# Kernel tuning notes

Hardware: AMD Instinct MI355X
Metric: run time of the kernel (lower is better)

The kernel has to match this reference:

```python
import jax, jax.numpy as jnp
import numpy as np

DIM = 1024
HEADS = 8
HEAD_DIM = DIM // HEADS
FFN = 4096
B, N = 32, 1024
EPS = 1e-5


def layer_norm(x, g, b):
    mu = jnp.mean(x, axis=-1, keepdims=True)
    var = jnp.mean(jnp.square(x - mu), axis=-1, keepdims=True)
    return (x - mu) * jax.lax.rsqrt(var + EPS) * g + b


def setup_inputs() -> dict:
    key = jax.random.key(0)
    ks = jax.random.split(key, 10)
    s = 0.02
    return {
        "x": jax.random.normal(ks[0], (B, N, DIM), dtype=jnp.float32),
        "haltingscore": jnp.zeros((B, N), dtype=jnp.float32),
        "Wq": jax.random.normal(ks[1], (DIM, DIM), dtype=jnp.float32) * s,
        "Wkv": jax.random.normal(ks[2], (DIM, 2 * DIM), dtype=jnp.float32) * s,
        "Wp": jax.random.normal(ks[3], (DIM, DIM), dtype=jnp.float32) * s,
        "bp": jnp.zeros((DIM,), dtype=jnp.float32),
        "W1": jax.random.normal(ks[4], (DIM, FFN), dtype=jnp.float32) * s,
        "b1": jnp.zeros((FFN,), dtype=jnp.float32),
        "W2": jax.random.normal(ks[5], (FFN, DIM), dtype=jnp.float32) * s,
        "b2": jnp.zeros((DIM,), dtype=jnp.float32),
        "ln1_g": jnp.ones((DIM,), dtype=jnp.float32),
        "ln1_b": jnp.zeros((DIM,), dtype=jnp.float32),
        "ln2_g": jnp.ones((DIM,), dtype=jnp.float32),
        "ln2_b": jnp.zeros((DIM,), dtype=jnp.float32),
    }


def reference(x, haltingscore, Wq, Wkv, Wp, bp, W1, b1, W2, b2,
              ln1_g, ln1_b, ln2_g, ln2_b):
    b, n, c = x.shape
    scale = HEAD_DIM ** -0.5
    # ---- EfficientAttention (explicit QK^T softmax V) ----
    q = (x @ Wq).reshape(b, n, HEADS, HEAD_DIM).transpose(0, 2, 1, 3)  # bhnd
    kv = (x @ Wkv).reshape(b, n, 2, HEADS, HEAD_DIM).transpose(2, 0, 3, 1, 4)
    k, v = kv[0], kv[1]                                               # bhnd
    attn = jax.nn.softmax(jnp.einsum('bhnd,bhmd->bhnm', q, k) * scale, axis=-1)
    o = jnp.einsum('bhnm,bhmd->bhnd', attn, v)
    o = o.transpose(0, 2, 1, 3).reshape(b, n, c)
    o = o @ Wp + bp
    attn_mean = jnp.mean(attn, axis=1)                                # (B, N, N)
    # ---- residual + LN1 ----
    h = layer_norm(x + o, ln1_g, ln1_b)
    # ---- FFN + residual + LN2 ----
    ff = jax.nn.relu(h @ W1 + b1) @ W2 + b2
    out = layer_norm(h + ff, ln2_g, ln2_b)
    # ---- halting score update ----
    a = jax.nn.softmax(jnp.sum(attn_mean, axis=1), axis=-1)           # (B, N)
    halting = haltingscore + a
    return (out, halting, a)
```

## Files before the change

kernel.cpp:

```cpp
#include <hip/hip_runtime.h>
#include <hip/hip_bf16.h>
#include <stdint.h>

#define DIMC 1024
#define HEADS 8
#define HDIM 128
#define FFND 4096
#define BATCH 32
#define SEQ 1024
#define SROWS (BATCH*SEQ)
#define QSTR 3072

typedef unsigned short u16;
typedef short short4v __attribute__((ext_vector_type(4)));
typedef short short8 __attribute__((ext_vector_type(8)));
typedef float f32x4 __attribute__((ext_vector_type(4)));
typedef __bf16 bf16x8 __attribute__((ext_vector_type(8)));

__device__ __forceinline__ u16 f2bf(float f) {
    union { float f; uint32_t u; } x{f};
    uint32_t r = x.u + 0x7FFFu + ((x.u >> 16) & 1u);
    return (u16)(r >> 16);
}
__device__ __forceinline__ float bf2f(u16 h) {
    union { uint32_t u; float f; } x;
    x.u = ((uint32_t)h) << 16;
    return x.f;
}

__device__ __forceinline__ f32x4 mfma16(short8 a, short8 b, f32x4 c) {
    return __builtin_amdgcn_mfma_f32_16x16x32_bf16(
        __builtin_bit_cast(bf16x8, a), __builtin_bit_cast(bf16x8, b), c, 0, 0, 0);
}

__device__ __forceinline__ void gload_lds16(const u16* g, u16* lds) {
    __builtin_amdgcn_global_load_lds(
        (const __attribute__((address_space(1))) uint32_t*)g,
        (__attribute__((address_space(3))) uint32_t*)lds, 16, 0, 0);
}

#define DPP_RORADD(x, ctrl) do {                                               \
    int _t = __builtin_amdgcn_mov_dpp(__builtin_bit_cast(int, (x)), (ctrl),    \
                                      0xf, 0xf, true);                         \
    (x) += __builtin_bit_cast(float, _t); } while (0)

__device__ __forceinline__ short8 p2frag(f32x4 p0, f32x4 p1, int lane) {
    uint32_t a, b, c, d;
    asm("v_cvt_pk_bf16_f32 %0, %1, %2" : "=v"(a) : "v"(p0[0]), "v"(p0[1]));
    asm("v_cvt_pk_bf16_f32 %0, %1, %2" : "=v"(b) : "v"(p0[2]), "v"(p0[3]));
    asm("v_cvt_pk_bf16_f32 %0, %1, %2" : "=v"(c) : "v"(p1[0]), "v"(p1[1]));
    asm("v_cvt_pk_bf16_f32 %0, %1, %2" : "=v"(d) : "v"(p1[2]), "v"(p1[3]));
    uint32_t ax = (uint32_t)__shfl_xor((int)a, 32);
    uint32_t bx = (uint32_t)__shfl_xor((int)b, 32);
    uint32_t cx = (uint32_t)__shfl_xor((int)c, 32);
    uint32_t dx = (uint32_t)__shfl_xor((int)d, 32);
    const bool up = (lane & 32) != 0;
    uint32_t P = up ? cx : a, Q = up ? c : ax;
    uint32_t R = up ? dx : b, S = up ? d : bx;
    uint32_t Px = (uint32_t)__shfl_xor((int)P, 16);
    uint32_t Qx = (uint32_t)__shfl_xor((int)Q, 16);
    uint32_t Rx = (uint32_t)__shfl_xor((int)R, 16);
    uint32_t Sx = (uint32_t)__shfl_xor((int)S, 16);
    const bool odd = (lane & 16) != 0;
    uint32_t w0 = odd ? Qx : P,  w1 = odd ? Sx : R;
    uint32_t w2 = odd ? Q  : Px, w3 = odd ? S  : Rx;
    union { uint32_t w[4]; short8 s; } u;
    u.w[0] = w0; u.w[1] = w1; u.w[2] = w2; u.w[3] = w3;
    return u.s;
}

__global__ __launch_bounds__(256) void k_cast(const float* __restrict__ in,
                                              u16* __restrict__ out, int n4) {
    int i = blockIdx.x * 256 + threadIdx.x;
    if (i < n4) {
        f32x4 v = ((const f32x4*)in)[i];
        uint32_t lo = f2bf(v[0]) | ((uint32_t)f2bf(v[1]) << 16);
        uint32_t hi = f2bf(v[2]) | ((uint32_t)f2bf(v[3]) << 16);
        ((uint2*)out)[i] = make_uint2(lo, hi);
    }
}

__global__ __launch_bounds__(256) void k_transpose_cast(const float* __restrict__ W,
                                                        u16* __restrict__ Wt,
                                                        int K, int N) {
    __shared__ u16 tile[32][33];
    int n0 = blockIdx.x * 32, k0 = blockIdx.y * 32;
    int tx = threadIdx.x, ty = threadIdx.y;
#pragma unroll
    for (int i = 0; i < 32; i += 8)
        tile[ty + i][tx] = f2bf(W[(size_t)(k0 + ty + i) * N + n0 + tx]);
    __syncthreads();
#pragma unroll
    for (int i = 0; i < 32; i += 8)
        Wt[(size_t)(n0 + ty + i) * K + k0 + tx] = tile[tx][ty + i];
}

template<bool OUT_BF16, bool RELU, bool BIAS, bool VSPLIT>
__global__ __launch_bounds__(512, 2) void k_gemm256(const u16* __restrict__ A,
                                                    const u16* __restrict__ Bt,
                                                    const float* __restrict__ bias,
                                                    void* __restrict__ C,
                                                    u16* __restrict__ Vt,
                                                    int M, int N, int K) {
    union Smem {
        struct { u16 A[4][8192]; u16 B[4][8192]; } k;
        u16 ob[64 * 264];
        float of[64 * 268];
        u16 vt[256 * 66];
    };
    __shared__ Smem smem;
    const int tid = threadIdx.x;
    const int lane = tid & 63, wv = tid >> 6;
    const int wm = wv >> 2, wn = wv & 3;
    const int l15 = lane & 15, lg = lane >> 4;
    const int gx = gridDim.x;
    const int nwg = gx * gridDim.y;
    const int id = blockIdx.y * gx + blockIdx.x;
    const int id2 = (id & 7) * (nwg >> 3) + (id >> 3);
    const int row0 = (id2 / gx) << 8, col0 = (id2 % gx) << 8;
    const int NT = K >> 5;

#define STAGE_A(tt) {                                                          \
    int _t = (tt);                                                             \
    _Pragma("unroll")                                                          \
    for (int i = 0; i < 2; ++i) {                                              \
        int blk = wv * 2 + i;                                                  \
        gload_lds16(A + (size_t)(row0 + blk * 16 + l15) * K + _t * 32 + lg * 8,\
                    &smem.k.A[_t & 3][blk * 512]);                             \
    } }
#define STAGE_B(tt) {                                                          \
    int _t = (tt);                                                             \
    _Pragma("unroll")                                                          \
    for (int i = 0; i < 2; ++i) {                                              \
        int blk = wv * 2 + i;                                                  \
        gload_lds16(Bt + (size_t)(col0 + blk * 16 + l15) * K + _t * 32 + lg * 8,\
                    &smem.k.B[_t & 3][blk * 512]);                             \
    } }

    STAGE_A(0); STAGE_B(0);
    STAGE_A(1); STAGE_B(1);
    STAGE_A(2); STAGE_B(2);

    f32x4 acc[8][4] = {};
    for (int t = 0; t < NT; ++t) {
        const int slot = t & 3;
        if (t <= NT - 3)      asm volatile("s_waitcnt vmcnt(8)" ::: "memory");
        else if (t == NT - 2) asm volatile("s_waitcnt vmcnt(4)" ::: "memory");
        else                  asm volatile("s_waitcnt vmcnt(0)" ::: "memory");
        __builtin_amdgcn_s_barrier();
        __builtin_amdgcn_sched_barrier(0);

        const u16* Ab = &smem.k.A[slot][(wm * 8) * 512];
        const u16* Bb = &smem.k.B[slot][(wn * 4) * 512];

        if (t + 3 < NT) STAGE_A(t + 3);
        short8 bf[4], af[4];
#pragma unroll
        for (int n = 0; n < 4; ++n) bf[n] = *(const short8*)(Bb + n * 512 + lane * 8);
#pragma unroll
        for (int m = 0; m < 4; ++m) af[m] = *(const short8*)(Ab + m * 512 + lane * 8);
        __builtin_amdgcn_s_setprio(1);
#pragma unroll
        for (int m = 0; m < 4; ++m)
#pragma unroll
            for (int n = 0; n < 4; ++n)
                acc[m][n] = mfma16(af[m], bf[n], acc[m][n]);
        __builtin_amdgcn_s_setprio(0);

        if (t + 3 < NT) STAGE_B(t + 3);
#pragma unroll
        for (int m = 0; m < 4; ++m) af[m] = *(const short8*)(Ab + (4 + m) * 512 + lane * 8);
        __builtin_amdgcn_s_setprio(1);
#pragma unroll
        for (int m = 0; m < 4; ++m)
#pragma unroll
            for (int n = 0; n < 4; ++n)
                acc[4 + m][n] = mfma16(af[m], bf[n], acc[4 + m][n]);
        __builtin_amdgcn_s_setprio(0);
    }
#undef STAGE_A
#undef STAGE_B

    const bool vpath = VSPLIT && (col0 >= 2048);
    __syncthreads();
#pragma unroll
    for (int s = 0; s < 4; ++s) {
        if (s) __syncthreads();
        if (wm == (s >> 1)) {
            const int mb4 = (s & 1) * 4;
#pragma unroll
            for (int mm = 0; mm < 4; ++mm)
#pragma unroll
                for (int n = 0; n < 4; ++n) {
                    int c = wn * 64 + n * 16 + l15;
                    float bv = BIAS ? bias[col0 + c] : 0.f;
#pragma unroll
                    for (int j = 0; j < 4; ++j) {
                        int lr = mm * 16 + lg * 4 + j;
                        float v = acc[mb4 + mm][n][j] + bv;
                        if (RELU) v = fmaxf(v, 0.f);
                        if (vpath)         smem.vt[c * 66 + lr] = f2bf(v);
                        else if (OUT_BF16) smem.ob[lr * 264 + c] = f2bf(v);
                        else               smem.of[lr * 268 + c] = v;
                    }
                }
        }
        __syncthreads();
        const int gr0 = row0 + s * 64;
        if (vpath) {
            const int bb = gr0 >> 10;
            const int mb = gr0 & 1023;
#pragma unroll
            for (int it = 0; it < 4; ++it) {
                int idx = it * 512 + tid;
                int dc = idx >> 3, mseg = idx & 7;
                int hh = (col0 - 2048 + dc) >> 7;
                int dd = (col0 - 2048 + dc) & 127;
                *(short8*)(Vt + ((size_t)(bb * 8 + hh)) * (HDIM * SEQ)
                              + (size_t)dd * SEQ + mb + mseg * 8) =
                    *(const short8*)(&smem.vt[dc * 66 + mseg * 8]);
            }
        } else if (OUT_BF16) {
#pragma unroll
            for (int it = 0; it < 4; ++it) {
                int idx = it * 512 + tid;
                int r = idx >> 5, seg = idx & 31;
                *(short8*)((u16*)C + (size_t)(gr0 + r) * N + col0 + seg * 8) =
                    *(const short8*)(&smem.ob[r * 264 + seg * 8]);
            }
        } else {
#pragma unroll
            for (int it = 0; it < 8; ++it) {
                int idx = it * 512 + tid;
                int r = idx >> 6, seg = idx & 63;
                *(f32x4*)((float*)C + (size_t)(gr0 + r) * N + col0 + seg * 4) =
                    *(const f32x4*)(&smem.of[r * 268 + seg * 4]);
            }
        }
    }
}

__global__ __launch_bounds__(256, 3) void k_attn(const u16* __restrict__ QKV,
                                                 const u16* __restrict__ Vt,
                                                 u16* __restrict__ O,
                                                 float* __restrict__ csp) {
    union Sm {
        u16 K2[2][8192];
        struct { u16 Kl[2][4096]; u16 Vl[2][4096]; } pb;
    };
    __shared__ Sm sm;
    __shared__ float cs[1024];
    const int id = blockIdx.x;
    const int id2 = (id & 7) * 256 + (id >> 3);
    const int qt = id2 & 7, bh = id2 >> 3;
    const int b = bh >> 3, h = bh & 7;
    const int tid = threadIdx.x, lane = tid & 63, wv = tid >> 6;
    const int l15 = lane & 15, lg = lane >> 4;

    for (int i = tid; i < 1024; i += 256) cs[i] = 0.f;

    const int q0 = qt * 128 + wv * 32;
    const u16* qbaseA = QKV + (size_t)(b * SEQ + q0 + l15) * QSTR + h * HDIM + lg * 8;
    const u16* qbaseB = qbaseA + (size_t)16 * QSTR;
    short8 qfA[4], qfB[4];
#pragma unroll
    for (int kk = 0; kk < 4; ++kk) {
        qfA[kk] = *(const short8*)(qbaseA + kk * 32);
        qfB[kk] = *(const short8*)(qbaseB + kk * 32);
    }
    const float CEXP = 0.12751743f;
    const u16* kbase = QKV + (size_t)(b * SEQ) * QSTR + 1024 + h * HDIM;
    const u16* vtb = Vt + (size_t)bh * HDIM * SEQ;

#define STAGE_K2(tt) { _Pragma("unroll")                                        \
    for (int i = 0; i < 4; ++i) {                                               \
        gload_lds16(kbase + (size_t)((tt) * 64 + wv * 16 + l15) * QSTR          \
                    + i * 32 + lg * 8, &sm.K2[(tt) & 1][(wv * 4 + i) * 512]); } }
#define STAGE_K(tt) { _Pragma("unroll")                                         \
    for (int i = 0; i < 2; ++i) { int c = wv * 2 + i;                           \
        gload_lds16(kbase + (size_t)((tt) * 32 + (c >> 2) * 16 + l15) * QSTR    \
                    + (c & 3) * 32 + lg * 8, &sm.pb.Kl[(tt) & 1][c * 512]); } }
#define STAGE_V(tt) { _Pragma("unroll")                                         \
    for (int i = 0; i < 2; ++i) { int c = wv * 2 + i;                           \
        gload_lds16(vtb + (size_t)(c * 16 + l15) * SEQ + (tt) * 32 + lg * 8,    \
                    &sm.pb.Vl[(tt) & 1][c * 512]); } }

    STAGE_K2(0);
    asm volatile("s_waitcnt vmcnt(0)" ::: "memory");
    __builtin_amdgcn_s_barrier();
    f32x4 rsA4 = {0.f, 0.f, 0.f, 0.f}, rsB4 = {0.f, 0.f, 0.f, 0.f};
    for (int t = 0; t < 16; ++t) {
        if (t < 15) STAGE_K2(t + 1);
        const u16* Kp = &sm.K2[t & 1][0];
        __builtin_amdgcn_s_setprio(1);
#pragma unroll
        for (int j = 0; j < 4; j += 2) {
            f32x4 s0 = {0.f,0.f,0.f,0.f}, s1 = {0.f,0.f,0.f,0.f};
            f32x4 s2 = {0.f,0.f,0.f,0.f}, s3 = {0.f,0.f,0.f,0.f};
#pragma unroll
            for (int kk = 0; kk < 4; ++kk) {
                short8 k0 = *(const short8*)(Kp + (j * 4 + kk) * 512 + lane * 8);
                short8 k1 = *(const short8*)(Kp + ((j + 1) * 4 + kk) * 512 + lane * 8);
                s0 = mfma16(k0, qfA[kk], s0);
                s1 = mfma16(k0, qfB[kk], s1);
                s2 = mfma16(k1, qfA[kk], s2);
                s3 = mfma16(k1, qfB[kk], s3);
            }
#pragma unroll
            for (int r = 0; r < 4; ++r) {
                rsA4[r] += __builtin_amdgcn_exp2f(s0[r] * CEXP)
                         + __builtin_amdgcn_exp2f(s2[r] * CEXP);
                rsB4[r] += __builtin_amdgcn_exp2f(s1[r] * CEXP)
                         + __builtin_amdgcn_exp2f(s3[r] * CEXP);
            }
        }
        __builtin_amdgcn_s_setprio(0);
        asm volatile("s_waitcnt vmcnt(0)" ::: "memory");
        __builtin_amdgcn_s_barrier();
    }
    float rsA = (rsA4[0] + rsA4[1]) + (rsA4[2] + rsA4[3]);
    float rsB = (rsB4[0] + rsB4[1]) + (rsB4[2] + rsB4[3]);
    rsA += __shfl_xor(rsA, 16); rsA += __shfl_xor(rsA, 32);
    rsB += __shfl_xor(rsB, 16); rsB += __shfl_xor(rsB, 32);
    const float invA = 1.f / rsA, invB = 1.f / rsB;

    STAGE_K(0); STAGE_V(0);
    asm volatile("s_waitcnt vmcnt(0)" ::: "memory");
    __builtin_amdgcn_s_barrier();
    f32x4 odA[8] = {}, odB[8] = {};
    for (int t = 0; t < 32; ++t) {
        const int m0 = t * 32;
        if (t < 31) { STAGE_K(t + 1); STAGE_V(t + 1); }
        const u16* Kp = &sm.pb.Kl[t & 1][0];
        f32x4 sA0 = {0.f,0.f,0.f,0.f}, sA1 = {0.f,0.f,0.f,0.f};
        f32x4 sB0 = {0.f,0.f,0.f,0.f}, sB1 = {0.f,0.f,0.f,0.f};
        __builtin_amdgcn_s_setprio(1);
#pragma unroll
        for (int kk = 0; kk < 4; ++kk) {
            short8 k0 = *(const short8*)(Kp + kk * 512 + lane * 8);
            short8 k1 = *(const short8*)(Kp + (4 + kk) * 512 + lane * 8);
            sA0 = mfma16(k0, qfA[kk], sA0);
            sA1 = mfma16(k1, qfA[kk], sA1);
            sB0 = mfma16(k0, qfB[kk], sB0);
            sB1 = mfma16(k1, qfB[kk], sB1);
        }
        __builtin_amdgcn_s_setprio(0);
        f32x4 pA0, pA1, pB0, pB1;
#pragma unroll
        for (int r = 0; r < 4; ++r) {
            pA0[r] = __builtin_amdgcn_exp2f(sA0[r] * CEXP) * invA;
            pA1[r] = __builtin_amdgcn_exp2f(sA1[r] * CEXP) * invA;
            pB0[r] = __builtin_amdgcn_exp2f(sB0[r] * CEXP) * invB;
            pB1[r] = __builtin_amdgcn_exp2f(sB1[r] * CEXP) * invB;
        }
        float csv[8];
#pragma unroll
        for (int r = 0; r < 4; ++r) {
            csv[r]     = pA0[r] + pB0[r];
            csv[4 + r] = pA1[r] + pB1[r];
        }
#pragma unroll
        for (int j2 = 0; j2 < 8; ++j2) {
            DPP_RORADD(csv[j2], 0x128);
            DPP_RORADD(csv[j2], 0x124);
            DPP_RORADD(csv[j2], 0x122);
            DPP_RORADD(csv[j2], 0x121);
        }
        float cval = csv[0];
        cval = (l15 == 1) ? csv[1] : cval;
        cval = (l15 == 2) ? csv[2] : cval;
        cval = (l15 == 3) ? csv[3] : cval;
        cval = (l15 == 4) ? csv[4] : cval;
        cval = (l15 == 5) ? csv[5] : cval;
        cval = (l15 == 6) ? csv[6] : cval;
        cval = (l15 == 7) ? csv[7] : cval;
        if (l15 < 8) {
            int mw = (l15 < 4) ? (lg * 4 + l15) : (16 + lg * 4 + (l15 - 4));
            atomicAdd(&cs[m0 + mw], cval);
        }
        short8 paA = p2frag(pA0, pA1, lane);
        short8 paB = p2frag(pB0, pB1, lane);
        const u16* Vb_ = &sm.pb.Vl[t & 1][0];
        __builtin_amdgcn_s_setprio(1);
#pragma unroll
        for (int db = 0; db < 8; ++db) {
            short8 vf = *(const short8*)(Vb_ + db * 512 + lane * 8);
            odA[db] = mfma16(paA, vf, odA[db]);
            odB[db] = mfma16(paB, vf, odB[db]);
        }
        __builtin_amdgcn_s_setprio(0);
        asm volatile("s_waitcnt vmcnt(0)" ::: "memory");
        __builtin_amdgcn_s_barrier();
    }
#undef STAGE_K2
#undef STAGE_K
#undef STAGE_V
    __syncthreads();
    u16* obA = O + (size_t)(b * SEQ + q0 + lg * 4) * DIMC + h * HDIM + l15;
    u16* obB = obA + (size_t)16 * DIMC;
#pragma unroll
    for (int db = 0; db < 8; ++db)
#pragma unroll
        for (int r = 0; r < 4; ++r) {
            obA[(size_t)r * DIMC + db * 16] = f2bf(odA[db][r]);
            obB[(size_t)r * DIMC + db * 16] = f2bf(odB[db][r]);
        }
    for (int m = tid; m < 1024; m += 256)
        csp[((size_t)bh * 8 + qt) * 1024 + m] = cs[m];
}

__global__ __launch_bounds__(256) void k_ln1(const float* __restrict__ xa,
                                             const u16* __restrict__ pj,
                                             const float* __restrict__ g,
                                             const float* __restrict__ bt,
                                             u16* __restrict__ ob) {
    const int row = blockIdx.x;
    const int t = threadIdx.x, lane = t & 63, wv = t >> 6;
    f32x4 va = ((const f32x4*)(xa + (size_t)row * DIMC))[t];
    short4v hv = ((const short4v*)(pj + (size_t)row * DIMC))[t];
    f32x4 s;
#pragma unroll
    for (int j = 0; j < 4; ++j) s[j] = va[j] + bf2f((u16)hv[j]);
    float sum = s[0] + s[1] + s[2] + s[3];
    float sq = s[0]*s[0] + s[1]*s[1] + s[2]*s[2] + s[3]*s[3];
#pragma unroll
    for (int o = 1; o < 64; o <<= 1) { sum += __shfl_xor(sum, o); sq += __shfl_xor(sq, o); }
    __shared__ float red[8];
    if (lane == 0) { red[wv] = sum; red[4 + wv] = sq; }
    __syncthreads();
    sum = red[0] + red[1] + red[2] + red[3];
    sq  = red[4] + red[5] + red[6] + red[7];
    float mu = sum * (1.f / DIMC);
    float rstd = rsqrtf(sq * (1.f / DIMC) - mu * mu + 1e-5f);
    f32x4 gg = ((const f32x4*)g)[t];
    f32x4 bb = ((const f32x4*)bt)[t];
    uint32_t lo, hi;
    float o0 = (s[0] - mu) * rstd * gg[0] + bb[0];
    float o1 = (s[1] - mu) * rstd * gg[1] + bb[1];
    float o2 = (s[2] - mu) * rstd * gg[2] + bb[2];
    float o3 = (s[3] - mu) * rstd * gg[3] + bb[3];
    lo = f2bf(o0) | ((uint32_t)f2bf(o1) << 16);
    hi = f2bf(o2) | ((uint32_t)f2bf(o3) << 16);
    ((uint2*)(ob + (size_t)row * DIMC))[t] = make_uint2(lo, hi);
}

__global__ __launch_bounds__(256) void k_ln2(const u16* __restrict__ xa,
                                             const u16* __restrict__ f2,
                                             const float* __restrict__ g,
                                             const float* __restrict__ bt,
                                             float* __restrict__ of) {
    const int row = blockIdx.x;
    const int t = threadIdx.x, lane = t & 63, wv = t >> 6;
    short4v hv = ((const short4v*)(xa + (size_t)row * DIMC))[t];
    short4v fv = ((const short4v*)(f2 + (size_t)row * DIMC))[t];
    f32x4 s;
#pragma unroll
    for (int j = 0; j < 4; ++j) s[j] = bf2f((u16)hv[j]) + bf2f((u16)fv[j]);
    float sum = s[0] + s[1] + s[2] + s[3];
    float sq = s[0]*s[0] + s[1]*s[1] + s[2]*s[2] + s[3]*s[3];
#pragma unroll
    for (int o = 1; o < 64; o <<= 1) { sum += __shfl_xor(sum, o); sq += __shfl_xor(sq, o); }
    __shared__ float red[8];
    if (lane == 0) { red[wv] = sum; red[4 + wv] = sq; }
    __syncthreads();
    sum = red[0] + red[1] + red[2] + red[3];
    sq  = red[4] + red[5] + red[6] + red[7];
    float mu = sum * (1.f / DIMC);
    float rstd = rsqrtf(sq * (1.f / DIMC) - mu * mu + 1e-5f);
    f32x4 gg = ((const f32x4*)g)[t];
    f32x4 bb = ((const f32x4*)bt)[t];
    f32x4 o4;
#pragma unroll
    for (int j = 0; j < 4; ++j) o4[j] = (s[j] - mu) * rstd * gg[j] + bb[j];
    ((f32x4*)(of + (size_t)row * DIMC))[t] = o4;
}

__global__ __launch_bounds__(256) void k_halt(const float* __restrict__ csp,
                                              const float* __restrict__ hs,
                                              float* __restrict__ halt_out,
                                              float* __restrict__ a_out) {
    const int b = blockIdx.x, t = threadIdx.x, lane = t & 63, wv = t >> 6;
    const float* base = csp + (size_t)b * 65536;
    float acc[4] = {0.f, 0.f, 0.f, 0.f};
    for (int s2 = 0; s2 < 64; ++s2) {
#pragma unroll
        for (int j = 0; j < 4; ++j) acc[j] += base[(size_t)s2 * 1024 + j * 256 + t];
    }
    float mx = -1e30f;
#pragma unroll
    for (int j = 0; j < 4; ++j) { acc[j] *= 0.125f; mx = fmaxf(mx, acc[j]); }
#pragma unroll
    for (int o = 1; o < 64; o <<= 1) mx = fmaxf(mx, __shfl_xor(mx, o));
    __shared__ float red[8];
    if (lane == 0) red[wv] = mx;
    __syncthreads();
    mx = fmaxf(fmaxf(red[0], red[1]), fmaxf(red[2], red[3]));
    float e[4]; float sum = 0.f;
#pragma unroll
    for (int j = 0; j < 4; ++j) { e[j] = __expf(acc[j] - mx); sum += e[j]; }
#pragma unroll
    for (int o = 1; o < 64; o <<= 1) sum += __shfl_xor(sum, o);
    if (lane == 0) red[4 + wv] = sum;
    __syncthreads();
    sum = red[4] + red[5] + red[6] + red[7];
    float inv = 1.f / sum;
#pragma unroll
    for (int j = 0; j < 4; ++j) {
        int m = j * 256 + t;
        float a = e[j] * inv;
        a_out[b * SEQ + m] = a;
        halt_out[b * SEQ + m] = hs[b * SEQ + m] + a;
    }
}

extern "C" void kernel_launch(void* const* d_in, const int* in_sizes, int n_in,
                              void* d_out, int out_size, void* d_ws, size_t ws_size,
                              hipStream_t stream) {
    (void)in_sizes; (void)n_in; (void)out_size; (void)ws_size;
    const float* x   = (const float*)d_in[0];
    const float* hs  = (const float*)d_in[1];
    const float* Wq  = (const float*)d_in[2];
    const float* Wkv = (const float*)d_in[3];
    const float* Wp  = (const float*)d_in[4];
    const float* bp  = (const float*)d_in[5];
    const float* W1  = (const float*)d_in[6];
    const float* b1  = (const float*)d_in[7];
    const float* W2  = (const float*)d_in[8];
    const float* b2  = (const float*)d_in[9];
    const float* g1  = (const float*)d_in[10];
    const float* be1 = (const float*)d_in[11];
    const float* g2  = (const float*)d_in[12];
    const float* be2 = (const float*)d_in[13];

    float* out = (float*)d_out;
    float* halt_out = out + (size_t)SROWS * DIMC;
    float* a_out = halt_out + SROWS;

    char* w = (char*)d_ws;
    const size_t MB = 1024 * 1024;
    u16*  xb    = (u16*)(w);
    u16*  qkv   = (u16*)(w + 64 * MB);
    u16*  Vt    = (u16*)(w + 256 * MB);
    u16*  WqkvT = (u16*)(w + 320 * MB);
    u16*  WpT   = (u16*)(w + 326 * MB);
    u16*  W1T   = (u16*)(w + 328 * MB);
    u16*  W2T   = (u16*)(w + 336 * MB);
    float* csp  = (float*)(w + 344 * MB);
    u16*  o_b   = (u16*)(w);
    u16*  projb = (u16*)(w + 64 * MB);
    u16*  hb    = (u16*)(w);
    u16*  ff1   = (u16*)(w + 64 * MB);
    u16*  ff2b  = (u16*)(w + 192 * MB);

    dim3 tb(32, 8);
    k_cast<<<SROWS * DIMC / 4 / 256, 256, 0, stream>>>(x, xb, SROWS * DIMC / 4);
    k_transpose_cast<<<dim3(DIMC / 32, DIMC / 32), tb, 0, stream>>>(Wq, WqkvT, DIMC, DIMC);
    k_transpose_cast<<<dim3(2 * DIMC / 32, DIMC / 32), tb, 0, stream>>>(
        Wkv, WqkvT + (size_t)DIMC * DIMC, DIMC, 2 * DIMC);
    k_transpose_cast<<<dim3(DIMC / 32, DIMC / 32), tb, 0, stream>>>(Wp, WpT, DIMC, DIMC);
    k_transpose_cast<<<dim3(FFND / 32, DIMC / 32), tb, 0, stream>>>(W1, W1T, DIMC, FFND);
    k_transpose_cast<<<dim3(DIMC / 32, FFND / 32), tb, 0, stream>>>(W2, W2T, FFND, DIMC);
    k_gemm256<true, false, false, true><<<dim3(QSTR / 256, SROWS / 256), 512, 0, stream>>>(
        xb, WqkvT, nullptr, qkv, Vt, SROWS, QSTR, DIMC);
    k_attn<<<2048, 256, 0, stream>>>(qkv, Vt, o_b, csp);
    k_gemm256<true, false, true, false><<<dim3(DIMC / 256, SROWS / 256), 512, 0, stream>>>(
        o_b, WpT, bp, projb, nullptr, SROWS, DIMC, DIMC);
    k_ln1<<<SROWS, 256, 0, stream>>>(x, projb, g1, be1, hb);
    for (int c = 0; c < 2; ++c) {
        const size_t ro = (size_t)c * 16384;
        k_gemm256<true, true, true, false><<<dim3(FFND / 256, 16384 / 256), 512, 0, stream>>>(
            hb + ro * DIMC, W1T, b1, ff1, nullptr, 16384, FFND, DIMC);
        k_gemm256<true, false, true, false><<<dim3(DIMC / 256, 16384 / 256), 512, 0, stream>>>(
            ff1, W2T, b2, ff2b, nullptr, 16384, DIMC, FFND);
        k_ln2<<<16384, 256, 0, stream>>>(hb + ro * DIMC, ff2b, g2, be2, out + ro * DIMC);
    }
    k_halt<<<BATCH, 256, 0, stream>>>(csp, hs, halt_out, a_out);
}
```

Measured before the change: 1.445 ms.

## Triple-buffer attention K/V staging and run FFN on full batch writing fp32 output

The attention kernel's K and V LDS staging goes from double to triple buffering. Loads are issued two tiles ahead, and each iteration now waits with a partial vmcnt at its start instead of draining all loads at its end, so global loads overlap more with MFMA work. The FFN path no longer runs as two half-batch chunks. The second GEMM writes fp32 directly into the output buffer and LN2 normalizes it in place, which drops the bf16 intermediate. The costs are more LDS per block, which may lower occupancy, and a larger ff1 workspace for the full batch (32768x4096 bf16, 256 MB), which may overlap other workspace regions.

```diff
diff --git a/kernel.cpp b/kernel.cpp
--- a/kernel.cpp
+++ b/kernel.cpp
@@ -245,8 +245,8 @@
                                                  u16* __restrict__ O,
                                                  float* __restrict__ csp) {
     union Sm {
-        u16 K2[2][8192];
-        struct { u16 Kl[2][4096]; u16 Vl[2][4096]; } pb;
+        u16 K2[3][8192];
+        struct { u16 Kl[3][4096]; u16 Vl[3][4096]; } pb;
     };
     __shared__ Sm sm;
     __shared__ float cs[1024];
@@ -268,30 +268,33 @@
         qfA[kk] = *(const short8*)(qbaseA + kk * 32);
         qfB[kk] = *(const short8*)(qbaseB + kk * 32);
     }
+    asm volatile("s_waitcnt vmcnt(0)" ::: "memory");
     const float CEXP = 0.12751743f;
     const u16* kbase = QKV + (size_t)(b * SEQ) * QSTR + 1024 + h * HDIM;
     const u16* vtb = Vt + (size_t)bh * HDIM * SEQ;
 
-#define STAGE_K2(tt) { _Pragma("unroll")                                        \
+#define STAGE_K2(tt, sl) { _Pragma("unroll")                                    \
     for (int i = 0; i < 4; ++i) {                                               \
         gload_lds16(kbase + (size_t)((tt) * 64 + wv * 16 + l15) * QSTR          \
-                    + i * 32 + lg * 8, &sm.K2[(tt) & 1][(wv * 4 + i) * 512]); } }
-#define STAGE_K(tt) { _Pragma("unroll")                                         \
+                    + i * 32 + lg * 8, &sm.K2[sl][(wv * 4 + i) * 512]); } }
+#define STAGE_K(tt, sl) { _Pragma("unroll")                                     \
     for (int i = 0; i < 2; ++i) { int c = wv * 2 + i;                           \
         gload_lds16(kbase + (size_t)((tt) * 32 + (c >> 2) * 16 + l15) * QSTR    \
-                    + (c & 3) * 32 + lg * 8, &sm.pb.Kl[(tt) & 1][c * 512]); } }
-#define STAGE_V(tt) { _Pragma("unroll")                                         \
+                    + (c & 3) * 32 + lg * 8, &sm.pb.Kl[sl][c * 512]); } }
+#define STAGE_V(tt, sl) { _Pragma("unroll")                                     \
     for (int i = 0; i < 2; ++i) { int c = wv * 2 + i;                           \
         gload_lds16(vtb + (size_t)(c * 16 + l15) * SEQ + (tt) * 32 + lg * 8,    \
-                    &sm.pb.Vl[(tt) & 1][c * 512]); } }
-
-    STAGE_K2(0);
-    asm volatile("s_waitcnt vmcnt(0)" ::: "memory");
-    __builtin_amdgcn_s_barrier();
+                    &sm.pb.Vl[sl][c * 512]); } }
+
+    STAGE_K2(0, 0); STAGE_K2(1, 1);
     f32x4 rsA4 = {0.f, 0.f, 0.f, 0.f}, rsB4 = {0.f, 0.f, 0.f, 0.f};
     for (int t = 0; t < 16; ++t) {
-        if (t < 15) STAGE_K2(t + 1);
-        const u16* Kp = &sm.K2[t & 1][0];
+        if (t < 15) asm volatile("s_waitcnt vmcnt(4)" ::: "memory");
+        else        asm volatile("s_waitcnt vmcnt(0)" ::: "memory");
+        __builtin_amdgcn_s_barrier();
+        __builtin_amdgcn_sched_barrier(0);
+        if (t < 14) STAGE_K2(t + 2, (t + 2) % 3);
+        const u16* Kp = &sm.K2[t % 3][0];
         __builtin_amdgcn_s_setprio(1);
 #pragma unroll
         for (int j = 0; j < 4; j += 2) {
@@ -315,8 +318,6 @@
             }
         }
         __builtin_amdgcn_s_setprio(0);
-        asm volatile("s_waitcnt vmcnt(0)" ::: "memory");
-        __builtin_amdgcn_s_barrier();
     }
     float rsA = (rsA4[0] + rsA4[1]) + (rsA4[2] + rsA4[3]);
     float rsB = (rsB4[0] + rsB4[1]) + (rsB4[2] + rsB4[3]);
@@ -324,14 +325,18 @@
     rsB += __shfl_xor(rsB, 16); rsB += __shfl_xor(rsB, 32);
     const float invA = 1.f / rsA, invB = 1.f / rsB;
 
-    STAGE_K(0); STAGE_V(0);
-    asm volatile("s_waitcnt vmcnt(0)" ::: "memory");
     __builtin_amdgcn_s_barrier();
+    STAGE_K(0, 0); STAGE_V(0, 0);
+    STAGE_K(1, 1); STAGE_V(1, 1);
     f32x4 odA[8] = {}, odB[8] = {};
     for (int t = 0; t < 32; ++t) {
         const int m0 = t * 32;
-        if (t < 31) { STAGE_K(t + 1); STAGE_V(t + 1); }
-        const u16* Kp = &sm.pb.Kl[t & 1][0];
+        if (t < 31) asm volatile("s_waitcnt vmcnt(4)" ::: "memory");
+        else        asm volatile("s_waitcnt vmcnt(0)" ::: "memory");
+        __builtin_amdgcn_s_barrier();
+        __builtin_amdgcn_sched_barrier(0);
+        if (t < 30) { STAGE_K(t + 2, (t + 2) % 3); STAGE_V(t + 2, (t + 2) % 3); }
+        const u16* Kp = &sm.pb.Kl[t % 3][0];
         f32x4 sA0 = {0.f,0.f,0.f,0.f}, sA1 = {0.f,0.f,0.f,0.f};
         f32x4 sB0 = {0.f,0.f,0.f,0.f}, sB1 = {0.f,0.f,0.f,0.f};
         __builtin_amdgcn_s_setprio(1);
@@ -380,7 +385,7 @@
         }
         short8 paA = p2frag(pA0, pA1, lane);
         short8 paB = p2frag(pB0, pB1, lane);
-        const u16* Vb_ = &sm.pb.Vl[t & 1][0];
+        const u16* Vb_ = &sm.pb.Vl[t % 3][0];
         __builtin_amdgcn_s_setprio(1);
 #pragma unroll
         for (int db = 0; db < 8; ++db) {
@@ -389,8 +394,6 @@
             odB[db] = mfma16(paB, vf, odB[db]);
         }
         __builtin_amdgcn_s_setprio(0);
-        asm volatile("s_waitcnt vmcnt(0)" ::: "memory");
-        __builtin_amdgcn_s_barrier();
     }
 #undef STAGE_K2
 #undef STAGE_K
@@ -445,17 +448,16 @@
 }
 
 __global__ __launch_bounds__(256) void k_ln2(const u16* __restrict__ xa,
-                                             const u16* __restrict__ f2,
                                              const float* __restrict__ g,
                                              const float* __restrict__ bt,
                                              float* __restrict__ of) {
     const int row = blockIdx.x;
     const int t = threadIdx.x, lane = t & 63, wv = t >> 6;
     short4v hv = ((const short4v*)(xa + (size_t)row * DIMC))[t];
-    short4v fv = ((const short4v*)(f2 + (size_t)row * DIMC))[t];
+    f32x4 fv = ((const f32x4*)(of + (size_t)row * DIMC))[t];
     f32x4 s;
 #pragma unroll
-    for (int j = 0; j < 4; ++j) s[j] = bf2f((u16)hv[j]) + bf2f((u16)fv[j]);
+    for (int j = 0; j < 4; ++j) s[j] = bf2f((u16)hv[j]) + fv[j];
     float sum = s[0] + s[1] + s[2] + s[3];
     float sq = s[0]*s[0] + s[1]*s[1] + s[2]*s[2] + s[3]*s[3];
 #pragma unroll
@@ -550,7 +552,6 @@
     u16*  projb = (u16*)(w + 64 * MB);
     u16*  hb    = (u16*)(w);
     u16*  ff1   = (u16*)(w + 64 * MB);
-    u16*  ff2b  = (u16*)(w + 192 * MB);
 
     dim3 tb(32, 8);
     k_cast<<<SROWS * DIMC / 4 / 256, 256, 0, stream>>>(x, xb, SROWS * DIMC / 4);
@@ -566,13 +567,10 @@
     k_gemm256<true, false, true, false><<<dim3(DIMC / 256, SROWS / 256), 512, 0, stream>>>(
         o_b, WpT, bp, projb, nullptr, SROWS, DIMC, DIMC);
     k_ln1<<<SROWS, 256, 0, stream>>>(x, projb, g1, be1, hb);
-    for (int c = 0; c < 2; ++c) {
-        const size_t ro = (size_t)c * 16384;
-        k_gemm256<true, true, true, false><<<dim3(FFND / 256, 16384 / 256), 512, 0, stream>>>(
-            hb + ro * DIMC, W1T, b1, ff1, nullptr, 16384, FFND, DIMC);
-        k_gemm256<true, false, true, false><<<dim3(DIMC / 256, 16384 / 256), 512, 0, stream>>>(
-            ff1, W2T, b2, ff2b, nullptr, 16384, DIMC, FFND);
-        k_ln2<<<16384, 256, 0, stream>>>(hb + ro * DIMC, ff2b, g2, be2, out + ro * DIMC);
-    }
+    k_gemm256<true, true, true, false><<<dim3(FFND / 256, SROWS / 256), 512, 0, stream>>>(
+        hb, W1T, b1, ff1, nullptr, SROWS, FFND, DIMC);
+    k_gemm256<false, false, true, false><<<dim3(DIMC / 256, SROWS / 256), 512, 0, stream>>>(
+        ff1, W2T, b2, out, nullptr, SROWS, DIMC, FFND);
+    k_ln2<<<SROWS, 256, 0, stream>>>(hb, g2, be2, out);
     k_halt<<<BATCH, 256, 0, stream>>>(csp, hs, halt_out, a_out);
 }
```

Measured after the change: 1.460 ms. About the same (+1.0%).
